# Kernel tuning notes

Hardware: AMD Instinct MI355X
Metric: run time of the kernel (lower is better)

The kernel has to match this reference:

```python
import jax, jax.numpy as jnp
import numpy as np

B, N, D, K = 128, 65536, 512, 5
RATIO = 0.5


def setup_inputs() -> dict:
    key = jax.random.key(0)
    k1, k2, k3 = jax.random.split(key, 3)
    return {
        "s_f": jax.random.normal(k1, (B, D), jnp.float32),
        "t_f": jax.random.normal(k2, (B, D), jnp.float32),
        "gallery": jax.random.normal(k3, (N, D), jnp.float32),
    }


def _l2_normalize(x):
    # F.normalize(p=2, dim=1) with eps=1e-12 clamp on the norm
    n = jnp.linalg.norm(x, axis=1, keepdims=True)
    return x / jnp.maximum(n, 1e-12)


def reference(s_f, t_f, gallery):
    m = int(D * RATIO)  # number of lowest-|product| channels kept per row
    t_n = _l2_normalize(t_f)        # [B, D]
    s_n = _l2_normalize(s_f)        # [B, D]
    g_n = _l2_normalize(gallery)    # [N, D]

    # cosine retrieval in float64, as in the original (t_f.double().mm(...))
    sims = jnp.einsum('bd,nd->bn', t_n.astype(jnp.float64), g_n.astype(jnp.float64))  # [B, N]
    _, top_idx = jax.lax.top_k(sims, K)  # descending sort, take first K -> [B, K]

    # gather the K nearest gallery rows for every batch sample
    neighbors = g_n[top_idx]                       # [B, K, D]
    dmat = jnp.abs(neighbors * s_n[:, None, :])    # [B, K, D]

    # per-row ascending sort; keep the m smallest channel indices
    low_idx = jnp.argsort(dmat, axis=-1)[..., :m]  # [B, K, m]

    # membership bitmask per (batch, k) row: channel c in its bottom-m set?
    member = jnp.zeros((B, K, D), dtype=bool)
    member = member.at[
        jnp.arange(B)[:, None, None],
        jnp.arange(K)[None, :, None],
        low_idx,
    ].set(True)

    # the original's iterative cat+unique+counts intersection == AND-reduce
    # of all membership sets, starting from the full index set arange(D)
    zero_out = jnp.all(member, axis=(0, 1))  # [D] bool

    # compactor mask: ones, with intersected filter indices zeroed
    mask = jnp.where(zero_out, 0.0, 1.0).astype(jnp.float32)  # [D]
    return mask
```

## Files before the change

kernel.cpp:

```cpp
#include <hip/hip_runtime.h>

#define B 128
#define N 65536
#define D 512
#define K 5
#define M 256
#define GPB 128
#define NBLK1 (N / GPB)
#define CHR 16
#define NCHK (GPB / CHR)

typedef __attribute__((ext_vector_type(8))) short short8;
typedef __attribute__((ext_vector_type(4))) float f32x4;
typedef __attribute__((address_space(1))) const unsigned char as1cu8;
typedef __attribute__((address_space(3))) unsigned char as3u8;

__device__ __forceinline__ unsigned int pack_bf2(float lo, float hi) {
    return __builtin_amdgcn_perm(__float_as_uint(hi), __float_as_uint(lo), 0x07060302u);
}

__device__ __forceinline__ void top5_insert(float v, int gi, float tv[K], int ti[K]) {
    if (v > tv[K - 1] || (v == tv[K - 1] && gi < ti[K - 1])) {
        tv[K - 1] = v; ti[K - 1] = gi;
        #pragma unroll
        for (int k = K - 1; k > 0; --k) {
            bool sw = (tv[k] > tv[k - 1]) || (tv[k] == tv[k - 1] && ti[k] < ti[k - 1]);
            if (sw) {
                float fv = tv[k]; tv[k] = tv[k - 1]; tv[k - 1] = fv;
                int fi = ti[k]; ti[k] = ti[k - 1]; ti[k - 1] = fi;
            }
        }
    }
}

__device__ __forceinline__ void pk_insert(float sp, float lst[K]) {
    if (sp > lst[K - 1]) {
        lst[K - 1] = sp;
        #pragma unroll
        for (int k = K - 1; k > 0; --k)
            if (lst[k] > lst[k - 1]) {
                float t2 = lst[k]; lst[k] = lst[k - 1]; lst[k - 1] = t2;
            }
    }
}

__global__ __launch_bounds__(1024) void k1_sims(const float* __restrict__ t_f,
                                                const float* __restrict__ gal,
                                                float2* __restrict__ partial) {
    __shared__ __align__(16) char gbuf[2][CHR * 2048];
    __shared__ __align__(16) float cbuf_c[8][256];
    __shared__ __align__(16) float cbuf_n[16];

    const int tid = threadIdx.x;
    const int blk = blockIdx.x;
    const int lane = tid & 63;
    const int w = tid >> 6;
    const int l15 = lane & 15;
    const int l4 = lane >> 4;
    const int bt = w & 7;
    const int kh = w >> 3;

    const char* gal_b = reinterpret_cast<const char*>(gal);
    const size_t rowbase = ((size_t)blk * GPB) * (D * 4);
    const int lsw = (lane * 16) ^ ((w & 7) << 4);

    auto DMA = [&](int c, int bi) {
        const char* s0 = gal_b + rowbase + ((size_t)c * CHR + w) * (D * 4) + lsw;
        char* d = &gbuf[bi][w * 2048];
        __builtin_amdgcn_global_load_lds((as1cu8*)s0, (as3u8*)d, 16, 0, 0);
        __builtin_amdgcn_global_load_lds((as1cu8*)(s0 + 1024), (as3u8*)(d + 1024), 16, 0, 0);
    };

    DMA(0, 0);

    short8 tfr[8];
    {
        const float* tp = t_f + (size_t)(bt * 16 + l15) * D + (kh * 8) * 32 + l4 * 8;
        #pragma unroll
        for (int j = 0; j < 8; ++j) {
            float4 a = *reinterpret_cast<const float4*>(tp + j * 32);
            float4 b = *reinterpret_cast<const float4*>(tp + j * 32 + 4);
            uint4 q;
            q.x = pack_bf2(a.x, a.y); q.y = pack_bf2(a.z, a.w);
            q.z = pack_bf2(b.x, b.y); q.w = pack_bf2(b.z, b.w);
            tfr[j] = *reinterpret_cast<short8*>(&q);
        }
    }

    float lst[K];
    #pragma unroll
    for (int k = 0; k < K; ++k) lst[k] = -1e30f;

    const int xr = (l15 & 7) << 4;

    for (int c = 0; c < NCHK; ++c) {
        const int bi = c & 1;
        __syncthreads();
        if (c + 1 < NCHK) DMA(c + 1, bi ^ 1);

        f32x4 acc = (f32x4)0.0f;
        float nrm = 0.0f;
        const char* gb = &gbuf[bi][0];
        #pragma unroll
        for (int j = 0; j < 8; ++j) {
            const int ks = kh * 8 + j;
            const int base = l15 * 2048 + ks * 128;
            float4 a0 = *reinterpret_cast<const float4*>(gb + base + ((l4 * 32) ^ xr));
            float4 a1 = *reinterpret_cast<const float4*>(gb + base + ((l4 * 32 + 16) ^ xr));
            nrm = fmaf(a0.x, a0.x, nrm); nrm = fmaf(a0.y, a0.y, nrm);
            nrm = fmaf(a0.z, a0.z, nrm); nrm = fmaf(a0.w, a0.w, nrm);
            nrm = fmaf(a1.x, a1.x, nrm); nrm = fmaf(a1.y, a1.y, nrm);
            nrm = fmaf(a1.z, a1.z, nrm); nrm = fmaf(a1.w, a1.w, nrm);
            uint4 q;
            q.x = pack_bf2(a0.x, a0.y); q.y = pack_bf2(a0.z, a0.w);
            q.z = pack_bf2(a1.x, a1.y); q.w = pack_bf2(a1.z, a1.w);
            short8 af = *reinterpret_cast<short8*>(&q);
            acc = __builtin_amdgcn_mfma_f32_16x16x32_bf16(af, tfr[j], acc, 0, 0, 0);
        }
        nrm += __shfl_xor(nrm, 16);
        nrm += __shfl_xor(nrm, 32);

        if (kh == 0) {
            *reinterpret_cast<f32x4*>(&cbuf_c[bt][lane * 4]) = acc;
            if (w == 0 && lane < CHR) cbuf_n[lane] = nrm;
        }

        asm volatile("s_waitcnt lgkmcnt(0)" ::: "memory");
        __builtin_amdgcn_sched_barrier(0);
        __builtin_amdgcn_s_barrier();
        __builtin_amdgcn_sched_barrier(0);

        if (kh == 1) {
            f32x4 c0 = *reinterpret_cast<const f32x4*>(&cbuf_c[bt][lane * 4]);
            float4 n0 = *reinterpret_cast<const float4*>(&cbuf_n[l4 * 4]);
            #pragma unroll
            for (int r = 0; r < 4; ++r) {
                float nown = __shfl(nrm, l4 * 4 + r);
                float s = (c0[r] + acc[r]) * rsqrtf(fmaxf(n0[r] + nown, 1e-24f));
                unsigned meta = (unsigned)(c * CHR + l4 * 4 + r);
                float sp = __uint_as_float((__float_as_uint(s) & 0xFFFFFF00u) | meta);
                pk_insert(sp, lst);
            }
        }
    }

    #pragma unroll
    for (int mk = 16; mk <= 32; mk <<= 1) {
        float inc[K];
        #pragma unroll
        for (int k = 0; k < K; ++k) inc[k] = __shfl_xor(lst[k], mk);
        #pragma unroll
        for (int k = 0; k < K; ++k) pk_insert(inc[k], lst);
    }

    if (kh == 1 && l4 == 0) {
        const int b = bt * 16 + l15;
        #pragma unroll
        for (int k = 0; k < K; ++k) {
            unsigned sp = __float_as_uint(lst[k]);
            int g = blk * GPB + (int)(sp & 0xFFu);
            partial[((size_t)b * NBLK1 + blk) * K + k] = make_float2(lst[k], __int_as_float(g));
        }
    }
}

__global__ __launch_bounds__(512) void k2_merge(const float2* __restrict__ partial,
                                                int* __restrict__ top_idx) {
    __shared__ float2 wlist[8][K];
    const int b = blockIdx.x;
    const int p = threadIdx.x;
    const int lane = p & 63;
    const int w = p >> 6;

    float mv[K]; int mi[K];
    #pragma unroll
    for (int k = 0; k < K; ++k) {
        float2 c = partial[((size_t)b * NBLK1 + p) * K + k];
        mv[k] = c.x; mi[k] = __float_as_int(c.y);
    }
    #pragma unroll
    for (int mk = 1; mk <= 32; mk <<= 1) {
        float ov[K]; int oi[K];
        #pragma unroll
        for (int k = 0; k < K; ++k) { ov[k] = __shfl_xor(mv[k], mk); oi[k] = __shfl_xor(mi[k], mk); }
        #pragma unroll
        for (int k = 0; k < K; ++k) top5_insert(ov[k], oi[k], mv, mi);
    }
    if (lane == 0) {
        #pragma unroll
        for (int k = 0; k < K; ++k) wlist[w][k] = make_float2(mv[k], __int_as_float(mi[k]));
    }
    __syncthreads();
    if (w == 0) {
        #pragma unroll
        for (int k = 0; k < K; ++k) { mv[k] = -1e30f; mi[k] = 0x7fffffff; }
        if (lane < 8) {
            #pragma unroll
            for (int k = 0; k < K; ++k) {
                float2 c = wlist[lane][k];
                mv[k] = c.x; mi[k] = __float_as_int(c.y);
            }
        }
        #pragma unroll
        for (int mk = 1; mk <= 4; mk <<= 1) {
            float ov[K]; int oi[K];
            #pragma unroll
            for (int k = 0; k < K; ++k) { ov[k] = __shfl_xor(mv[k], mk); oi[k] = __shfl_xor(mi[k], mk); }
            #pragma unroll
            for (int k = 0; k < K; ++k) top5_insert(ov[k], oi[k], mv, mi);
        }
        if (lane == 0) {
            #pragma unroll
            for (int k = 0; k < K; ++k) top_idx[b * K + k] = mi[k];
        }
    }
}

__global__ __launch_bounds__(512) void k3_member(const float* __restrict__ s_f,
                                                 const float* __restrict__ gal,
                                                 const int* __restrict__ top_idx,
                                                 unsigned long long* __restrict__ bkmask) {
    __shared__ __align__(16) float pS[D];
    const int p = threadIdx.x;
    const int bk = blockIdx.x;
    const int b = bk / K;
    const int row = top_idx[bk];
    float pv = fabsf(gal[(size_t)row * D + p] * s_f[(size_t)b * D + p]);
    pS[p] = pv;
    __syncthreads();
    int cnt = 0;
    const float4* p4 = reinterpret_cast<const float4*>(pS);
    #pragma unroll 4
    for (int j = 0; j < D / 4; ++j) {
        float4 o = p4[j];
        cnt += (o.x < pv || (o.x == pv && (4 * j + 0) < p)) ? 1 : 0;
        cnt += (o.y < pv || (o.y == pv && (4 * j + 1) < p)) ? 1 : 0;
        cnt += (o.z < pv || (o.z == pv && (4 * j + 2) < p)) ? 1 : 0;
        cnt += (o.w < pv || (o.w == pv && (4 * j + 3) < p)) ? 1 : 0;
    }
    unsigned long long bm = __ballot(cnt < M);
    if ((p & 63) == 0) bkmask[(size_t)bk * 8 + (p >> 6)] = bm;
}

__global__ __launch_bounds__(512) void k4_final(const unsigned long long* __restrict__ bkmask,
                                                float* __restrict__ out) {
    __shared__ unsigned long long red[64][8];
    const int t = threadIdx.x;
    {
        const int word = t & 7, seg = t >> 3;
        unsigned long long acc = ~0ull;
        #pragma unroll
        for (int i = 0; i < 10; ++i)
            acc &= bkmask[(size_t)(seg * 10 + i) * 8 + word];
        red[seg][word] = acc;
    }
    __syncthreads();
    const int word = t >> 6, bit = t & 63;
    unsigned long long m = ~0ull;
    #pragma unroll 8
    for (int seg = 0; seg < 64; ++seg) m &= red[seg][word];
    out[t] = ((m >> bit) & 1ull) ? 0.0f : 1.0f;
}

extern "C" void kernel_launch(void* const* d_in, const int* in_sizes, int n_in,
                              void* d_out, int out_size, void* d_ws, size_t ws_size,
                              hipStream_t stream) {
    (void)in_sizes; (void)n_in; (void)out_size; (void)ws_size;
    const float* s_f = (const float*)d_in[0];
    const float* t_f = (const float*)d_in[1];
    const float* gal = (const float*)d_in[2];
    float* out = (float*)d_out;

    char* ws = (char*)d_ws;
    const size_t off_partial = 0;
    const size_t off_topidx  = off_partial + 2621440;
    const size_t off_bkmask  = off_topidx + 2560;

    float2* partial = (float2*)(ws + off_partial);
    int* top_idx = (int*)(ws + off_topidx);
    unsigned long long* bkmask = (unsigned long long*)(ws + off_bkmask);

    hipLaunchKernelGGL(k1_sims, dim3(NBLK1), dim3(1024), 0, stream, t_f, gal, partial);
    hipLaunchKernelGGL(k2_merge, dim3(B), dim3(512), 0, stream, partial, top_idx);
    hipLaunchKernelGGL(k3_member, dim3(B * K), dim3(512), 0, stream, s_f, gal, top_idx, bkmask);
    hipLaunchKernelGGL(k4_final, dim3(1), dim3(512), 0, stream, bkmask, out);
}
```

Measured before the change: 108.0 us.

## Retile similarity kernel: stream D in chunks, split batch across paired blocks

The similarity kernel now holds all 128 gallery rows of a slab as 8 MFMA accumulators per wave and streams the D dimension in 32-column chunks, double-buffered through LDS. The split-K across two wave halves and its per-chunk LDS exchange and barrier are gone. Each slab is now handled by two 256-thread blocks, one per half of the batch, so each wave keeps its full t_f fragment in registers. The cost is that every gallery slab is fetched twice from global memory, relying on the paired blocks hitting in cache. Register pressure also rises from the 8 accumulators and 16 bf16 fragments.

```diff
diff --git a/kernel.cpp b/kernel.cpp
--- a/kernel.cpp
+++ b/kernel.cpp
@@ -6,9 +6,9 @@
 #define K 5
 #define M 256
 #define GPB 128
-#define NBLK1 (N / GPB)
-#define CHR 16
-#define NCHK (GPB / CHR)
+#define NBLKG (N / GPB)
+#define BK 32
+#define NCH (D / BK)
 
 typedef __attribute__((ext_vector_type(8))) short short8;
 typedef __attribute__((ext_vector_type(4))) float f32x4;
@@ -44,103 +44,100 @@
     }
 }
 
-__global__ __launch_bounds__(1024) void k1_sims(const float* __restrict__ t_f,
-                                                const float* __restrict__ gal,
-                                                float2* __restrict__ partial) {
-    __shared__ __align__(16) char gbuf[2][CHR * 2048];
-    __shared__ __align__(16) float cbuf_c[8][256];
-    __shared__ __align__(16) float cbuf_n[16];
+__global__ __launch_bounds__(256) void k1_sims(const float* __restrict__ t_f,
+                                               const float* __restrict__ gal,
+                                               float2* __restrict__ partial) {
+    __shared__ __align__(16) char gbuf[2][GPB * 128];
 
     const int tid = threadIdx.x;
-    const int blk = blockIdx.x;
+    const int gb = blockIdx.x >> 1;
+    const int bgrp = blockIdx.x & 1;
     const int lane = tid & 63;
     const int w = tid >> 6;
     const int l15 = lane & 15;
     const int l4 = lane >> 4;
-    const int bt = w & 7;
-    const int kh = w >> 3;
 
     const char* gal_b = reinterpret_cast<const char*>(gal);
-    const size_t rowbase = ((size_t)blk * GPB) * (D * 4);
-    const int lsw = (lane * 16) ^ ((w & 7) << 4);
-
-    auto DMA = [&](int c, int bi) {
-        const char* s0 = gal_b + rowbase + ((size_t)c * CHR + w) * (D * 4) + lsw;
-        char* d = &gbuf[bi][w * 2048];
-        __builtin_amdgcn_global_load_lds((as1cu8*)s0, (as3u8*)d, 16, 0, 0);
-        __builtin_amdgcn_global_load_lds((as1cu8*)(s0 + 1024), (as3u8*)(d + 1024), 16, 0, 0);
-    };
+    const size_t slab = (size_t)gb * GPB * 2048;
+
+#define DMA(ch, bi) do { \
+        _Pragma("unroll") \
+        for (int i_ = 0; i_ < 4; ++i_) { \
+            const int r0_ = w * 32 + i_ * 8 + (lane >> 3); \
+            const char* s_ = gal_b + slab + (size_t)r0_ * 2048 + (ch) * 128 \
+                             + (((lane & 7) * 16) ^ ((r0_ & 7) << 4)); \
+            char* d_ = &gbuf[bi][(w * 32 + i_ * 8) * 128]; \
+            __builtin_amdgcn_global_load_lds((as1cu8*)s_, (as3u8*)d_, 16, 0, 0); \
+        } \
+    } while (0)
 
     DMA(0, 0);
 
-    short8 tfr[8];
+    short8 tfr[16];
     {
-        const float* tp = t_f + (size_t)(bt * 16 + l15) * D + (kh * 8) * 32 + l4 * 8;
-        #pragma unroll
-        for (int j = 0; j < 8; ++j) {
-            float4 a = *reinterpret_cast<const float4*>(tp + j * 32);
-            float4 b = *reinterpret_cast<const float4*>(tp + j * 32 + 4);
+        const float* tp = t_f + (size_t)(bgrp * 64 + w * 16 + l15) * D + l4 * 8;
+        #pragma unroll
+        for (int ks = 0; ks < 16; ++ks) {
+            float4 a = *reinterpret_cast<const float4*>(tp + ks * 32);
+            float4 b = *reinterpret_cast<const float4*>(tp + ks * 32 + 4);
             uint4 q;
             q.x = pack_bf2(a.x, a.y); q.y = pack_bf2(a.z, a.w);
             q.z = pack_bf2(b.x, b.y); q.w = pack_bf2(b.z, b.w);
-            tfr[j] = *reinterpret_cast<short8*>(&q);
-        }
-    }
-
+            tfr[ks] = *reinterpret_cast<short8*>(&q);
+        }
+    }
+
+    f32x4 acc[8];
+    float nrm[8];
+    #pragma unroll
+    for (int gg = 0; gg < 8; ++gg) { acc[gg] = (f32x4)0.0f; nrm[gg] = 0.0f; }
     float lst[K];
     #pragma unroll
     for (int k = 0; k < K; ++k) lst[k] = -1e30f;
 
-    const int xr = (l15 & 7) << 4;
-
-    for (int c = 0; c < NCHK; ++c) {
-        const int bi = c & 1;
-        __syncthreads();
-        if (c + 1 < NCHK) DMA(c + 1, bi ^ 1);
-
-        f32x4 acc = (f32x4)0.0f;
-        float nrm = 0.0f;
-        const char* gb = &gbuf[bi][0];
-        #pragma unroll
-        for (int j = 0; j < 8; ++j) {
-            const int ks = kh * 8 + j;
-            const int base = l15 * 2048 + ks * 128;
-            float4 a0 = *reinterpret_cast<const float4*>(gb + base + ((l4 * 32) ^ xr));
-            float4 a1 = *reinterpret_cast<const float4*>(gb + base + ((l4 * 32 + 16) ^ xr));
-            nrm = fmaf(a0.x, a0.x, nrm); nrm = fmaf(a0.y, a0.y, nrm);
-            nrm = fmaf(a0.z, a0.z, nrm); nrm = fmaf(a0.w, a0.w, nrm);
-            nrm = fmaf(a1.x, a1.x, nrm); nrm = fmaf(a1.y, a1.y, nrm);
-            nrm = fmaf(a1.z, a1.z, nrm); nrm = fmaf(a1.w, a1.w, nrm);
+    __syncthreads();
+
+    #pragma unroll
+    for (int ch = 0; ch < NCH; ++ch) {
+        const int bi = ch & 1;
+        if (ch + 1 < NCH) DMA(ch + 1, bi ^ 1);
+
+        const char* gbp = &gbuf[bi][0];
+        #pragma unroll
+        for (int gg = 0; gg < 8; ++gg) {
+            const int row = gg * 16 + l15;
+            const int base = row * 128;
+            const int xr = (row & 7) << 4;
+            float4 a0 = *reinterpret_cast<const float4*>(gbp + base + ((l4 * 32) ^ xr));
+            float4 a1 = *reinterpret_cast<const float4*>(gbp + base + ((l4 * 32 + 16) ^ xr));
+            nrm[gg] = fmaf(a0.x, a0.x, nrm[gg]); nrm[gg] = fmaf(a0.y, a0.y, nrm[gg]);
+            nrm[gg] = fmaf(a0.z, a0.z, nrm[gg]); nrm[gg] = fmaf(a0.w, a0.w, nrm[gg]);
+            nrm[gg] = fmaf(a1.x, a1.x, nrm[gg]); nrm[gg] = fmaf(a1.y, a1.y, nrm[gg]);
+            nrm[gg] = fmaf(a1.z, a1.z, nrm[gg]); nrm[gg] = fmaf(a1.w, a1.w, nrm[gg]);
             uint4 q;
             q.x = pack_bf2(a0.x, a0.y); q.y = pack_bf2(a0.z, a0.w);
             q.z = pack_bf2(a1.x, a1.y); q.w = pack_bf2(a1.z, a1.w);
             short8 af = *reinterpret_cast<short8*>(&q);
-            acc = __builtin_amdgcn_mfma_f32_16x16x32_bf16(af, tfr[j], acc, 0, 0, 0);
-        }
-        nrm += __shfl_xor(nrm, 16);
-        nrm += __shfl_xor(nrm, 32);
-
-        if (kh == 0) {
-            *reinterpret_cast<f32x4*>(&cbuf_c[bt][lane * 4]) = acc;
-            if (w == 0 && lane < CHR) cbuf_n[lane] = nrm;
-        }
-
-        asm volatile("s_waitcnt lgkmcnt(0)" ::: "memory");
-        __builtin_amdgcn_sched_barrier(0);
-        __builtin_amdgcn_s_barrier();
-        __builtin_amdgcn_sched_barrier(0);
-
-        if (kh == 1) {
-            f32x4 c0 = *reinterpret_cast<const f32x4*>(&cbuf_c[bt][lane * 4]);
-            float4 n0 = *reinterpret_cast<const float4*>(&cbuf_n[l4 * 4]);
-            #pragma unroll
-            for (int r = 0; r < 4; ++r) {
-                float nown = __shfl(nrm, l4 * 4 + r);
-                float s = (c0[r] + acc[r]) * rsqrtf(fmaxf(n0[r] + nown, 1e-24f));
-                unsigned meta = (unsigned)(c * CHR + l4 * 4 + r);
-                float sp = __uint_as_float((__float_as_uint(s) & 0xFFFFFF00u) | meta);
-                pk_insert(sp, lst);
-            }
+            acc[gg] = __builtin_amdgcn_mfma_f32_16x16x32_bf16(af, tfr[ch], acc[gg], 0, 0, 0);
+        }
+        __syncthreads();
+    }
+
+    #pragma unroll
+    for (int gg = 0; gg < 8; ++gg) {
+        nrm[gg] += __shfl_xor(nrm[gg], 16);
+        nrm[gg] += __shfl_xor(nrm[gg], 32);
+    }
+
+    #pragma unroll
+    for (int gg = 0; gg < 8; ++gg) {
+        #pragma unroll
+        for (int r = 0; r < 4; ++r) {
+            float nr = __shfl(nrm[gg], l4 * 4 + r);
+            float s = acc[gg][r] * rsqrtf(fmaxf(nr, 1e-24f));
+            unsigned meta = (unsigned)(gg * 16 + l4 * 4 + r);
+            float sp = __uint_as_float((__float_as_uint(s) & 0xFFFFFF00u) | meta);
+            pk_insert(sp, lst);
         }
     }
 
@@ -153,15 +150,16 @@
         for (int k = 0; k < K; ++k) pk_insert(inc[k], lst);
     }
 
-    if (kh == 1 && l4 == 0) {
-        const int b = bt * 16 + l15;
+    if (l4 == 0) {
+        const int b = bgrp * 64 + w * 16 + l15;
         #pragma unroll
         for (int k = 0; k < K; ++k) {
             unsigned sp = __float_as_uint(lst[k]);
-            int g = blk * GPB + (int)(sp & 0xFFu);
-            partial[((size_t)b * NBLK1 + blk) * K + k] = make_float2(lst[k], __int_as_float(g));
-        }
-    }
+            int g = gb * GPB + (int)(sp & 0xFFu);
+            partial[((size_t)b * NBLKG + gb) * K + k] = make_float2(lst[k], __int_as_float(g));
+        }
+    }
+#undef DMA
 }
 
 __global__ __launch_bounds__(512) void k2_merge(const float2* __restrict__ partial,
@@ -175,7 +173,7 @@
     float mv[K]; int mi[K];
     #pragma unroll
     for (int k = 0; k < K; ++k) {
-        float2 c = partial[((size_t)b * NBLK1 + p) * K + k];
+        float2 c = partial[((size_t)b * NBLKG + p) * K + k];
         mv[k] = c.x; mi[k] = __float_as_int(c.y);
     }
     #pragma unroll
@@ -280,7 +278,7 @@
     int* top_idx = (int*)(ws + off_topidx);
     unsigned long long* bkmask = (unsigned long long*)(ws + off_bkmask);
 
-    hipLaunchKernelGGL(k1_sims, dim3(NBLK1), dim3(1024), 0, stream, t_f, gal, partial);
+    hipLaunchKernelGGL(k1_sims, dim3(NBLKG * 2), dim3(256), 0, stream, t_f, gal, partial);
     hipLaunchKernelGGL(k2_merge, dim3(B), dim3(512), 0, stream, partial, top_idx);
     hipLaunchKernelGGL(k3_member, dim3(B * K), dim3(512), 0, stream, s_f, gal, top_idx, bkmask);
     hipLaunchKernelGGL(k4_final, dim3(1), dim3(512), 0, stream, bkmask, out);
```

New measurement: 116.6 us. 1.08x slower.
